# Kernel tuning notes

Measured on AMD Instinct MI355X. Metric: run time of the kernel, lower is better.

## Reference

```python
import jax, jax.numpy as jnp
import numpy as np

B, S, D = 4, 4096, 128

def setup_inputs() -> dict:
    key = jax.random.key(0)
    kq, kk, kv = jax.random.split(key, 3)
    q = jax.random.normal(kq, (B, S, D), dtype=jnp.float32)
    k = jax.random.normal(kk, (B, S, D), dtype=jnp.float32)
    v = jax.random.normal(kv, (B, S, D), dtype=jnp.float32)
    return {"q": q, "k": k, "v": v}

def reference(q, k, v):
    d_model = q.shape[-1]
    scale = 1.0 / jnp.sqrt(jnp.asarray(d_model, q.dtype))
    # [B, S, S] scores
    scores = jnp.einsum('bqd,bkd->bqk', q, k) * scale
    s = q.shape[1]
    causal = jnp.tril(jnp.ones((s, s), dtype=bool))
    neg_inf = jnp.asarray(-jnp.inf, scores.dtype)
    scores = jnp.where(causal[None, :, :], scores, neg_inf)
    attn = jax.nn.softmax(scores, axis=-1)
    return jnp.einsum('bqk,bkd->bqd', attn, v)
```

## Files before the change

### kernel.cpp

```cpp
#include <hip/hip_runtime.h>


#define B_   4
#define S_   4096
#define D_   128
#define BN   64
#define NT_  64
#define QT_  32
#define NCHB 128
#define BLOB_SHORTS 16384
#define MASKVAL (-1.0e30f)
#define DEFER_THR 8.0f

#define CHK_INIT {1,1,1,1, 2,2,2,2,2, 3,3,3,3,3, 4,4,4,4,4, 5,5,5,5, 6,6,6,6,6, 7,7,7, 8}
#define BASE_INIT {127,126,125,124, 122,120,118,116,114, 111,108,105,102,99, \
                   95,91,87,83,79, 74,69,64,59, 53,47,41,35,29, 22,15,8, 0}

__constant__ short CHKd[32]  = CHK_INIT;
__constant__ short BASEd[32] = BASE_INIT;
constexpr short CHKh[32] = CHK_INIT;
constexpr short BASEh[32] = BASE_INIT;
constexpr int nchb_calc() { int s = 0; for (int t = 0; t < QT_; ++t) s += CHKh[t]; return s; }
static_assert(nchb_calc() == NCHB, "chunk count mismatch");
constexpr bool base_ok() {
    for (int t = 0; t < QT_; ++t) {
        int s = 0;
        for (int tt = t + 1; tt < QT_; ++tt) s += CHKh[tt];
        if (s != BASEh[t]) return false;
    }
    return true;
}
static_assert(base_ok(), "BASE table mismatch");

typedef __attribute__((ext_vector_type(8))) short bf16x8;
typedef __attribute__((ext_vector_type(4))) float f32x4;

__device__ __forceinline__ short f2bf(float x) {
    unsigned u = __builtin_bit_cast(unsigned, x);
    unsigned r = (u + 0x7fffu + ((u >> 16) & 1u)) >> 16;
    return (short)r;
}
__device__ __forceinline__ float ex2(float x) { return __builtin_amdgcn_exp2f(x); }
__device__ __forceinline__ unsigned cvtpk(float lo, float hi) {
    unsigned r;
    asm("v_cvt_pk_bf16_f32 %0, %1, %2" : "=v"(r) : "v"(lo), "v"(hi));
    return r;
}
__device__ __forceinline__ void gl_lds16(const short* g, short* l) {
    __builtin_amdgcn_global_load_lds(
        (const __attribute__((address_space(1))) unsigned int*)g,
        (__attribute__((address_space(3))) unsigned int*)l, 16, 0, 0);
}

__global__ __launch_bounds__(256) void prep(const float* __restrict__ Qg,
                                            const float* __restrict__ Kg,
                                            const float* __restrict__ Vg,
                                            short* __restrict__ Qbf,
                                            short* __restrict__ KV)
{
    __shared__ short vt[64][40];
    const int id  = blockIdx.x;
    const int tid = threadIdx.x;
    const float SC = 0.12751740f;

    if (id < 1024) {
        const int b = id & 3, tile = (id >> 2) & 63, q4 = id >> 8;
        const int n = q4 * 16 + (tid >> 4);
        const int G = tid & 15;
        const size_t rowoff = ((size_t)b * S_ + (size_t)tile * 64 + n) * D_ + G * 8;
        short* blob = KV + (size_t)(b * NT_ + tile) * BLOB_SHORTS;
        {
            float4 a = *reinterpret_cast<const float4*>(Qg + rowoff);
            float4 c = *reinterpret_cast<const float4*>(Qg + rowoff + 4);
            bf16x8 v;
            v[0] = f2bf(a.x * SC); v[1] = f2bf(a.y * SC); v[2] = f2bf(a.z * SC); v[3] = f2bf(a.w * SC);
            v[4] = f2bf(c.x * SC); v[5] = f2bf(c.y * SC); v[6] = f2bf(c.z * SC); v[7] = f2bf(c.w * SC);
            *reinterpret_cast<bf16x8*>(Qbf + rowoff) = v;
        }
        {
            float4 a = *reinterpret_cast<const float4*>(Kg + rowoff);
            float4 c = *reinterpret_cast<const float4*>(Kg + rowoff + 4);
            bf16x8 v;
            v[0] = f2bf(a.x); v[1] = f2bf(a.y); v[2] = f2bf(a.z); v[3] = f2bf(a.w);
            v[4] = f2bf(c.x); v[5] = f2bf(c.y); v[6] = f2bf(c.z); v[7] = f2bf(c.w);
            const int p = (G & 8) | ((G & 7) ^ (n & 7));
            *reinterpret_cast<bf16x8*>(blob + n * 128 + p * 8) = v;
        }
    } else {
        const int u = id - 1024;
        const int b = u & 3, tile = (u >> 2) & 63, dq = u >> 8;
        short* blob = KV + (size_t)(b * NT_ + tile) * BLOB_SHORTS;
        {
            const int n = tid >> 2, c8 = tid & 3;
            const size_t off = ((size_t)b * S_ + (size_t)tile * 64 + n) * D_ + dq * 32 + c8 * 8;
            float4 a = *reinterpret_cast<const float4*>(Vg + off);
            float4 c = *reinterpret_cast<const float4*>(Vg + off + 4);
            bf16x8 v;
            v[0] = f2bf(a.x); v[1] = f2bf(a.y); v[2] = f2bf(a.z); v[3] = f2bf(a.w);
            v[4] = f2bf(c.x); v[5] = f2bf(c.y); v[6] = f2bf(c.z); v[7] = f2bf(c.w);
            *reinterpret_cast<bf16x8*>(&vt[n][c8 * 8]) = v;
        }
        __syncthreads();
        {
            const int dl = tid >> 3, G = tid & 7;
            const int d  = dq * 32 + dl;
            bf16x8 g;
#pragma unroll
            for (int i = 0; i < 8; ++i) g[i] = vt[G * 8 + i][dl];
            const int p = G ^ (d & 7);
            *reinterpret_cast<bf16x8*>(blob + 8192 + d * 64 + p * 8) = g;
        }
    }
}

template<bool SPLIT>
__global__ __launch_bounds__(512, 4) void fa_fwd(const short* __restrict__ Qbf,
                                                 const short* __restrict__ KV,
                                                 float* __restrict__ Og,
                                                 unsigned* __restrict__ Op,
                                                 float* __restrict__ Ml)
{
    __shared__ short lkv[2][BLOB_SHORTS];

    const int tid  = threadIdx.x;
    const int wv   = tid >> 6;
    const int lane = tid & 63;
    const int m    = lane & 15;
    const int quad = lane >> 4;
    const int m7   = m & 7;

    int batch, t, lo, hi, chunk_id;
    {
        const int id = blockIdx.x;
        batch = id & 3;
        int u = id >> 2;
        if (SPLIT) {
            int tt = QT_ - 1, base = 0, rt;
            for (;;) { rt = CHKd[tt]; if (u < base + rt) break; base += rt; --tt; }
            t = tt;
            const int r  = u - base;
            const int nk = 2 * t + 2;
            lo = r * nk / rt;
            hi = (r + 1) * nk / rt;
            chunk_id = batch * NCHB + u;
        } else {
            t  = QT_ - 1 - u;
            lo = 0; hi = 2 * t + 2; chunk_id = 0;
        }
        if (lo >= hi) return;
    }

    bf16x8 qf[4];
    {
        const short* qp = Qbf + ((size_t)batch * S_ + (size_t)t * 128 + wv * 16 + m) * D_ + quad * 8;
#pragma unroll
        for (int c = 0; c < 4; ++c)
            qf[c] = *reinterpret_cast<const bf16x8*>(qp + c * 32);
    }

    f32x4 acc[8];
#pragma unroll
    for (int i = 0; i < 8; ++i) acc[i] = (f32x4){0.f, 0.f, 0.f, 0.f};
    float mrun = MASKVAL, lrun = 0.f;

    const size_t tilebase = (size_t)batch * NT_ * BLOB_SHORTS;
    const int qtop = t * 128 + wv * 16 + 15;
#define STAGE(KT, BUF) do {                                                   \
        const short* g_ = KV + tilebase + (size_t)(KT) * BLOB_SHORTS + tid * 8;\
        short* l_ = (BUF) + tid * 8;                                          \
        _Pragma("unroll")                                                     \
        for (int c_ = 0; c_ < 4; ++c_)                                        \
            gl_lds16(g_ + c_ * 4096, l_ + c_ * 4096);                         \
    } while (0)

    STAGE(lo, lkv[0]);

    for (int kt = lo; kt < hi; ++kt) {
        const short* cur = lkv[(kt - lo) & 1];
        short* nxt = lkv[(kt - lo + 1) & 1];
        __syncthreads();
        if (kt + 1 < hi) STAGE(kt + 1, nxt);

        if (kt * 64 > qtop) continue;

        const short* lk = cur;
        const short* lv = cur + 8192;

        f32x4 st[4];
#pragma unroll
        for (int nt = 0; nt < 4; ++nt) st[nt] = (f32x4){0.f, 0.f, 0.f, 0.f};
        __builtin_amdgcn_s_setprio(1);
#pragma unroll
        for (int c = 0; c < 4; ++c) {
            const int p = ((c >> 1) * 8) | ((((c & 1) * 4) | quad) ^ m7);
#pragma unroll
            for (int nt = 0; nt < 4; ++nt) {
                bf16x8 kf = *reinterpret_cast<const bf16x8*>(lk + nt * 2048 + m * 128 + p * 8);
                st[nt] = __builtin_amdgcn_mfma_f32_16x16x32_bf16(kf, qf[c], st[nt], 0, 0, 0);
            }
        }
        __builtin_amdgcn_s_setprio(0);

        if (kt >= 2 * t) {
            const int kbase = (kt - 2 * t) * 64;
            const int qloc  = wv * 16 + m;
#pragma unroll
            for (int nt = 0; nt < 4; ++nt)
#pragma unroll
                for (int r = 0; r < 4; ++r)
                    if (kbase + nt * 16 + quad * 4 + r > qloc) st[nt][r] = MASKVAL;
        }

        float t0 = fmaxf(fmaxf(st[0][0], st[0][1]), fmaxf(st[0][2], st[0][3]));
        float t1 = fmaxf(fmaxf(st[1][0], st[1][1]), fmaxf(st[1][2], st[1][3]));
        float t2 = fmaxf(fmaxf(st[2][0], st[2][1]), fmaxf(st[2][2], st[2][3]));
        float t3 = fmaxf(fmaxf(st[3][0], st[3][1]), fmaxf(st[3][2], st[3][3]));
        float mx = fmaxf(fmaxf(t0, t1), fmaxf(t2, t3));
        if (__any(mx - mrun > DEFER_THR)) {
            float mw = fmaxf(mx, __shfl_xor(mx, 16));
            mw = fmaxf(mw, __shfl_xor(mw, 32));
            const float mnew = fmaxf(mrun, mw);
            const float al   = ex2(mrun - mnew);
            mrun = mnew;
            lrun *= al;
#pragma unroll
            for (int r = 0; r < 4; ++r) {
                float alq = __shfl(al, quad * 4 + r);
#pragma unroll
                for (int ct = 0; ct < 8; ++ct) acc[ct][r] *= alq;
            }
        }
        float sum = 0.f;
#pragma unroll
        for (int nt = 0; nt < 4; ++nt)
#pragma unroll
            for (int r = 0; r < 4; ++r) {
                float pv = ex2(st[nt][r] - mrun);
                st[nt][r] = pv;
                sum += pv;
            }
        lrun += sum;

        const int srcA = ((quad & 1) << 5) + m;
        const int srcB = srcA + 16;
        const bool loq = quad < 2;
#pragma unroll
        for (int ks = 0; ks < 2; ++ks) {
            unsigned pk0 = cvtpk(st[2 * ks][0],     st[2 * ks][1]);
            unsigned pk1 = cvtpk(st[2 * ks][2],     st[2 * ks][3]);
            unsigned pk2 = cvtpk(st[2 * ks + 1][0], st[2 * ks + 1][1]);
            unsigned pk3 = cvtpk(st[2 * ks + 1][2], st[2 * ks + 1][3]);
            unsigned w0a = __shfl((int)pk0, srcA);
            unsigned w0b = __shfl((int)pk2, srcA);
            unsigned w1a = __shfl((int)pk1, srcA);
            unsigned w1b = __shfl((int)pk3, srcA);
            unsigned w2a = __shfl((int)pk0, srcB);
            unsigned w2b = __shfl((int)pk2, srcB);
            unsigned w3a = __shfl((int)pk1, srcB);
            unsigned w3b = __shfl((int)pk3, srcB);
            int4 wi;
            wi.x = (int)(loq ? w0a : w0b);
            wi.y = (int)(loq ? w1a : w1b);
            wi.z = (int)(loq ? w2a : w2b);
            wi.w = (int)(loq ? w3a : w3b);
            bf16x8 pf = __builtin_bit_cast(bf16x8, wi);
            const int p = (ks * 4 + quad) ^ m7;
            __builtin_amdgcn_s_setprio(1);
#pragma unroll
            for (int ct = 0; ct < 8; ++ct) {
                bf16x8 vf = *reinterpret_cast<const bf16x8*>(lv + ct * 1024 + m * 64 + p * 8);
                acc[ct] = __builtin_amdgcn_mfma_f32_16x16x32_bf16(pf, vf, acc[ct], 0, 0, 0);
            }
            __builtin_amdgcn_s_setprio(0);
        }
    }
#undef STAGE

    lrun += __shfl_xor(lrun, 16);
    lrun += __shfl_xor(lrun, 32);

    const int row0 = wv * 16 + quad * 4;
    if (SPLIT) {
        unsigned* ob = Op + (size_t)chunk_id * (128 * 64);
#pragma unroll
        for (int r = 0; r < 4; ++r) {
            uint4 w;
            w.x = cvtpk(acc[0][r], acc[1][r]);
            w.y = cvtpk(acc[2][r], acc[3][r]);
            w.z = cvtpk(acc[4][r], acc[5][r]);
            w.w = cvtpk(acc[6][r], acc[7][r]);
            *reinterpret_cast<uint4*>(ob + (row0 + r) * 64 + m * 4) = w;
        }
        if (lane < 16) {
            float* mlb = Ml + (size_t)chunk_id * (128 * 2) + (wv * 16 + lane) * 2;
            mlb[0] = mrun;
            mlb[1] = lrun;
        }
    } else {
        const float inv = 1.0f / lrun;
        const size_t obase = ((size_t)batch * S_ + (size_t)t * 128 + row0) * D_;
#pragma unroll
        for (int r = 0; r < 4; ++r) {
            float invq = __shfl(inv, quad * 4 + r);
#pragma unroll
            for (int ct = 0; ct < 8; ++ct)
                Og[obase + (size_t)r * D_ + ct * 16 + m] = acc[ct][r] * invq;
        }
    }
}

__global__ __launch_bounds__(256) void fa_merge(const unsigned* __restrict__ Op,
                                                const float* __restrict__ Ml,
                                                float* __restrict__ Og)
{
    const int x   = blockIdx.x;
    const int btq = x >> 4;
    const int oct = x & 15;
    const int t   = btq & (QT_ - 1);
    const int b   = btq >> 5;
    const int rt  = CHKd[t];
    const int cbase = b * NCHB + BASEd[t];
    const int row = oct * 8 + (threadIdx.x >> 5);
    const int g   = threadIdx.x & 31;

    float mr_[8], lr_[8];
    float mg = MASKVAL;
#pragma unroll
    for (int r = 0; r < 8; ++r)
        if (r < rt) {
            float2 ml2 = *reinterpret_cast<const float2*>(
                Ml + (size_t)(cbase + r) * (128 * 2) + row * 2);
            mr_[r] = ml2.x;
            lr_[r] = ml2.y;
            mg = fmaxf(mg, mr_[r]);
        }
    float l = 0.f;
    float a0 = 0.f, a1 = 0.f, a2 = 0.f, a3 = 0.f;
#pragma unroll
    for (int r = 0; r < 8; ++r)
        if (r < rt) {
            float w = ex2(mr_[r] - mg);
            l += lr_[r] * w;
            uint2 pk = *reinterpret_cast<const uint2*>(
                Op + (size_t)(cbase + r) * (128 * 64) + row * 64 + g * 2);
            a0 += w * __builtin_bit_cast(float, pk.x << 16);
            a1 += w * __builtin_bit_cast(float, pk.x & 0xffff0000u);
            a2 += w * __builtin_bit_cast(float, pk.y << 16);
            a3 += w * __builtin_bit_cast(float, pk.y & 0xffff0000u);
        }
    const float inv = 1.0f / l;
    float* og = Og + (size_t)btq * (128 * D_) + row * D_;
    const int d0 = 64 * (g & 1) + (g >> 1);
    og[d0]      = a0 * inv;
    og[d0 + 16] = a1 * inv;
    og[d0 + 32] = a2 * inv;
    og[d0 + 48] = a3 * inv;
}

extern "C" void kernel_launch(void* const* d_in, const int* in_sizes, int n_in,
                              void* d_out, int out_size, void* d_ws, size_t ws_size,
                              hipStream_t stream) {
    const float* q = (const float*)d_in[0];
    const float* k = (const float*)d_in[1];
    const float* v = (const float*)d_in[2];
    float* o = (float*)d_out;

    const size_t QBF_BYTES = (size_t)B_ * S_ * D_ * 2;
    const size_t KV_BYTES  = (size_t)B_ * NT_ * BLOB_SHORTS * 2;
    const size_t PREFIX    = QBF_BYTES + KV_BYTES;
    const int    NCH       = B_ * NCHB;
    const size_t O_BYTES   = (size_t)NCH * 128 * 64 * 4;
    const size_t ML_BYTES  = (size_t)NCH * 128 * 2 * 4;
    const size_t NEEDED    = PREFIX + O_BYTES + ML_BYTES;

    char* ws = (char*)d_ws;
    short* Qbf = (short*)ws;
    short* KV  = (short*)(ws + QBF_BYTES);

    prep<<<dim3(2048), 256, 0, stream>>>(q, k, v, Qbf, KV);

    if (ws_size >= NEEDED) {
        unsigned* Op = (unsigned*)(ws + PREFIX);
        float* Ml = (float*)(ws + PREFIX + O_BYTES);
        fa_fwd<true><<<dim3(NCH), 512, 0, stream>>>(Qbf, KV, nullptr, Op, Ml);
        fa_merge<<<dim3(B_ * QT_ * 16), 256, 0, stream>>>(Op, Ml, o);
    } else {
        fa_fwd<false><<<dim3(B_ * QT_), 512, 0, stream>>>(Qbf, KV, o, nullptr, nullptr);
    }
}
```

Baseline: 115.2 us.

## Fuse split-K merge into attention kernel via last-block atomic counter

Removes the separate merge kernel: each split chunk increments a per-(batch, query-tile) atomic counter after writing its partial output. The block that arrives last merges all partial results and writes the final output. Counters are zeroed in the prep kernel. This saves one kernel launch and its tail gap, but puts the merge work onto the final arriving blocks and adds fences and atomics.

```diff
diff --git a/kernel.cpp b/kernel.cpp
--- a/kernel.cpp
+++ b/kernel.cpp
@@ -56,12 +56,15 @@
                                             const float* __restrict__ Kg,
                                             const float* __restrict__ Vg,
                                             short* __restrict__ Qbf,
-                                            short* __restrict__ KV)
+                                            short* __restrict__ KV,
+                                            int* __restrict__ Cnt)
 {
     __shared__ short vt[64][40];
     const int id  = blockIdx.x;
     const int tid = threadIdx.x;
     const float SC = 0.12751740f;
+
+    if (id == 0 && tid < B_ * QT_) Cnt[tid] = 0;
 
     if (id < 1024) {
         const int b = id & 3, tile = (id >> 2) & 63, q4 = id >> 8;
@@ -118,9 +121,11 @@
                                                  const short* __restrict__ KV,
                                                  float* __restrict__ Og,
                                                  unsigned* __restrict__ Op,
-                                                 float* __restrict__ Ml)
+                                                 float* __restrict__ Ml,
+                                                 int* __restrict__ Cnt)
 {
     __shared__ short lkv[2][BLOB_SHORTS];
+    __shared__ int lastf;
 
     const int tid  = threadIdx.x;
     const int wv   = tid >> 6;
@@ -129,7 +134,7 @@
     const int quad = lane >> 4;
     const int m7   = m & 7;
 
-    int batch, t, lo, hi, chunk_id;
+    int batch, t, lo, hi, chunk_id, rt_chunks;
     {
         const int id = blockIdx.x;
         batch = id & 3;
@@ -138,6 +143,7 @@
             int tt = QT_ - 1, base = 0, rt;
             for (;;) { rt = CHKd[tt]; if (u < base + rt) break; base += rt; --tt; }
             t = tt;
+            rt_chunks = rt;
             const int r  = u - base;
             const int nk = 2 * t + 2;
             lo = r * nk / rt;
@@ -145,7 +151,7 @@
             chunk_id = batch * NCHB + u;
         } else {
             t  = QT_ - 1 - u;
-            lo = 0; hi = 2 * t + 2; chunk_id = 0;
+            lo = 0; hi = 2 * t + 2; chunk_id = 0; rt_chunks = 1;
         }
         if (lo >= hi) return;
     }
@@ -296,6 +302,54 @@
             mlb[0] = mrun;
             mlb[1] = lrun;
         }
+
+        __threadfence();
+        if (tid == 0) {
+            int old = atomicAdd(&Cnt[batch * QT_ + t], 1);
+            lastf = (old == rt_chunks - 1);
+        }
+        __syncthreads();
+        if (!lastf) return;
+        __threadfence();
+
+        const int cb = batch * NCHB + BASEd[t];
+        const int rt = rt_chunks;
+        for (int i = tid; i < 4096; i += 512) {
+            const int row = i >> 5;
+            const int g   = i & 31;
+            float mr_[8], lr_[8];
+            float mg = MASKVAL;
+#pragma unroll
+            for (int r = 0; r < 8; ++r)
+                if (r < rt) {
+                    float2 ml2 = *reinterpret_cast<const float2*>(
+                        Ml + (size_t)(cb + r) * (128 * 2) + row * 2);
+                    mr_[r] = ml2.x;
+                    lr_[r] = ml2.y;
+                    mg = fmaxf(mg, mr_[r]);
+                }
+            float l = 0.f;
+            float a0 = 0.f, a1 = 0.f, a2 = 0.f, a3 = 0.f;
+#pragma unroll
+            for (int r = 0; r < 8; ++r)
+                if (r < rt) {
+                    float w = ex2(mr_[r] - mg);
+                    l += lr_[r] * w;
+                    uint2 pk = *reinterpret_cast<const uint2*>(
+                        Op + (size_t)(cb + r) * (128 * 64) + row * 64 + g * 2);
+                    a0 += w * __builtin_bit_cast(float, pk.x << 16);
+                    a1 += w * __builtin_bit_cast(float, pk.x & 0xffff0000u);
+                    a2 += w * __builtin_bit_cast(float, pk.y << 16);
+                    a3 += w * __builtin_bit_cast(float, pk.y & 0xffff0000u);
+                }
+            const float inv = 1.0f / l;
+            float* og = Og + ((size_t)batch * S_ + (size_t)t * 128 + row) * D_;
+            const int d0 = 64 * (g & 1) + (g >> 1);
+            og[d0]      = a0 * inv;
+            og[d0 + 16] = a1 * inv;
+            og[d0 + 32] = a2 * inv;
+            og[d0 + 48] = a3 * inv;
+        }
     } else {
         const float inv = 1.0f / lrun;
         const size_t obase = ((size_t)batch * S_ + (size_t)t * 128 + row0) * D_;
@@ -307,54 +361,6 @@
                 Og[obase + (size_t)r * D_ + ct * 16 + m] = acc[ct][r] * invq;
         }
     }
-}
-
-__global__ __launch_bounds__(256) void fa_merge(const unsigned* __restrict__ Op,
-                                                const float* __restrict__ Ml,
-                                                float* __restrict__ Og)
-{
-    const int x   = blockIdx.x;
-    const int btq = x >> 4;
-    const int oct = x & 15;
-    const int t   = btq & (QT_ - 1);
-    const int b   = btq >> 5;
-    const int rt  = CHKd[t];
-    const int cbase = b * NCHB + BASEd[t];
-    const int row = oct * 8 + (threadIdx.x >> 5);
-    const int g   = threadIdx.x & 31;
-
-    float mr_[8], lr_[8];
-    float mg = MASKVAL;
-#pragma unroll
-    for (int r = 0; r < 8; ++r)
-        if (r < rt) {
-            float2 ml2 = *reinterpret_cast<const float2*>(
-                Ml + (size_t)(cbase + r) * (128 * 2) + row * 2);
-            mr_[r] = ml2.x;
-            lr_[r] = ml2.y;
-            mg = fmaxf(mg, mr_[r]);
-        }
-    float l = 0.f;
-    float a0 = 0.f, a1 = 0.f, a2 = 0.f, a3 = 0.f;
-#pragma unroll
-    for (int r = 0; r < 8; ++r)
-        if (r < rt) {
-            float w = ex2(mr_[r] - mg);
-            l += lr_[r] * w;
-            uint2 pk = *reinterpret_cast<const uint2*>(
-                Op + (size_t)(cbase + r) * (128 * 64) + row * 64 + g * 2);
-            a0 += w * __builtin_bit_cast(float, pk.x << 16);
-            a1 += w * __builtin_bit_cast(float, pk.x & 0xffff0000u);
-            a2 += w * __builtin_bit_cast(float, pk.y << 16);
-            a3 += w * __builtin_bit_cast(float, pk.y & 0xffff0000u);
-        }
-    const float inv = 1.0f / l;
-    float* og = Og + (size_t)btq * (128 * D_) + row * D_;
-    const int d0 = 64 * (g & 1) + (g >> 1);
-    og[d0]      = a0 * inv;
-    og[d0 + 16] = a1 * inv;
-    og[d0 + 32] = a2 * inv;
-    og[d0 + 48] = a3 * inv;
 }
 
 extern "C" void kernel_launch(void* const* d_in, const int* in_sizes, int n_in,
@@ -371,20 +377,21 @@
     const int    NCH       = B_ * NCHB;
     const size_t O_BYTES   = (size_t)NCH * 128 * 64 * 4;
     const size_t ML_BYTES  = (size_t)NCH * 128 * 2 * 4;
-    const size_t NEEDED    = PREFIX + O_BYTES + ML_BYTES;
+    const size_t CNT_BYTES = (size_t)(B_ * QT_) * 4;
+    const size_t NEEDED    = PREFIX + O_BYTES + ML_BYTES + CNT_BYTES;
 
     char* ws = (char*)d_ws;
     short* Qbf = (short*)ws;
     short* KV  = (short*)(ws + QBF_BYTES);
-
-    prep<<<dim3(2048), 256, 0, stream>>>(q, k, v, Qbf, KV);
+    unsigned* Op = (unsigned*)(ws + PREFIX);
+    float* Ml = (float*)(ws + PREFIX + O_BYTES);
+    int* Cnt = (int*)(ws + PREFIX + O_BYTES + ML_BYTES);
+
+    prep<<<dim3(2048), 256, 0, stream>>>(q, k, v, Qbf, KV, Cnt);
 
     if (ws_size >= NEEDED) {
-        unsigned* Op = (unsigned*)(ws + PREFIX);
-        float* Ml = (float*)(ws + PREFIX + O_BYTES);
-        fa_fwd<true><<<dim3(NCH), 512, 0, stream>>>(Qbf, KV, nullptr, Op, Ml);
-        fa_merge<<<dim3(B_ * QT_ * 16), 256, 0, stream>>>(Op, Ml, o);
+        fa_fwd<true><<<dim3(NCH), 512, 0, stream>>>(Qbf, KV, o, Op, Ml, Cnt);
     } else {
-        fa_fwd<false><<<dim3(B_ * QT_), 512, 0, stream>>>(Qbf, KV, o, nullptr, nullptr);
-    }
-}
+        fa_fwd<false><<<dim3(B_ * QT_), 512, 0, stream>>>(Qbf, KV, o, nullptr, nullptr, nullptr);
+    }
+}
```

New measurement: 263.2 us. +128.4%, slower.
